# Optimization experiments

Hardware: AMD Instinct MI355X
Metric: run time of the kernel (lower is better)

## Reference

```python
import jax, jax.numpy as jnp
import numpy as np


def setup_inputs() -> dict:
    key = jax.random.key(0)
    ks = jax.random.split(key, 5)
    B, Td, Te, D, U = 8, 64, 1024, 256, 128
    scale = 1.0 / np.sqrt(D)
    return {
        "decoder_output": jax.random.normal(ks[0], (B, Td, D), jnp.float32),
        "encoder_output": jax.random.normal(ks[1], (B, Te, D), jnp.float32),
        "W1": jax.random.normal(ks[2], (D, U), jnp.float32) * scale,
        "b1": jnp.zeros((U,), jnp.float32),
        "W2": jax.random.normal(ks[3], (D, U), jnp.float32) * scale,
        "b2": jnp.zeros((U,), jnp.float32),
        "V": jax.random.normal(ks[4], (U, 1), jnp.float32) * (1.0 / np.sqrt(U)),
        "bV": jnp.zeros((1,), jnp.float32),
    }


def reference(decoder_output, encoder_output, W1, b1, W2, b2, V, bV):
    # Original loops over decoder timesteps (state unused) -> fully vectorized.
    # w_enc: [B,Te,U] computed ONCE (original wastefully recomputes per step;
    # math is identical).
    w_enc = jnp.einsum("bsd,du->bsu", encoder_output, W1) + b1
    w_dec = jnp.einsum("btd,du->btu", decoder_output, W2) + b2
    # additive score: [B,Td,Te]
    score = (
        jnp.einsum("btsu,u->bts", jnp.tanh(w_enc[:, None, :, :] + w_dec[:, :, None, :]), V[:, 0])
        + bV[0]
    )
    attn = jax.nn.softmax(score, axis=-1)  # softmax over encoder time
    context = jnp.einsum("bts,bsd->btd", attn, encoder_output)  # [B,Td,D]
    return context
```

## Files before the change

kernel.cpp:

```cpp
#include <hip/hip_runtime.h>
#include <math.h>

#define NB   8
#define TD   64
#define TE   1024
#define DDIM 256
#define UDIM 128
#define NSC  16
#define SCHUNK (TE / NSC)

__device__ __forceinline__ float rcp_fast(float x) {
    return __builtin_amdgcn_rcpf(x);
}

__global__ __launch_bounds__(256) void k_compute_E(
    const float* __restrict__ enc, const float* __restrict__ dec,
    const float* __restrict__ W1, const float* __restrict__ b1,
    const float* __restrict__ W2, const float* __restrict__ b2,
    float* __restrict__ E_enc, float* __restrict__ E_dec)
{
    __shared__ alignas(16) float ldsT[DDIM][20];

    const int blk = blockIdx.x;
    const float *W, *bias, *in;
    float *out;
    if (blk < 512) {
        in   = enc + (size_t)blk * 16 * DDIM;
        W    = W1;  bias = b1;
        out  = E_enc + (size_t)blk * 16 * UDIM;
    } else {
        const int bd = blk - 512;
        in   = dec + (size_t)bd * 16 * DDIM;
        W    = W2;  bias = b2;
        out  = E_dec + (size_t)bd * 16 * UDIM;
    }

    const int tid = threadIdx.x;
    for (int i = tid; i < 16 * DDIM; i += 256) {
        const int r = i >> 8;
        const int d = i & 255;
        ldsT[d][r] = in[i];
    }
    __syncthreads();

    const int u0 = (tid & 63) * 2;
    const int r0 = (tid >> 6) * 4;

    float acc[4][2];
    #pragma unroll
    for (int r = 0; r < 4; ++r) { acc[r][0] = 0.f; acc[r][1] = 0.f; }

    #pragma unroll 4
    for (int d = 0; d < DDIM; ++d) {
        const float2 w2 = *(const float2*)(W + d * UDIM + u0);
        const float4 a4 = *(const float4*)(&ldsT[d][r0]);
        acc[0][0] = fmaf(a4.x, w2.x, acc[0][0]); acc[0][1] = fmaf(a4.x, w2.y, acc[0][1]);
        acc[1][0] = fmaf(a4.y, w2.x, acc[1][0]); acc[1][1] = fmaf(a4.y, w2.y, acc[1][1]);
        acc[2][0] = fmaf(a4.z, w2.x, acc[2][0]); acc[2][1] = fmaf(a4.z, w2.y, acc[2][1]);
        acc[3][0] = fmaf(a4.w, w2.x, acc[3][0]); acc[3][1] = fmaf(a4.w, w2.y, acc[3][1]);
    }

    const float k2l2e = 2.0f * 1.4426950408889634f;
    const float bb0 = bias[u0], bb1 = bias[u0 + 1];
    #pragma unroll
    for (int r = 0; r < 4; ++r) {
        const float e0 = exp2f((acc[r][0] + bb0) * k2l2e);
        const float e1 = exp2f((acc[r][1] + bb1) * k2l2e);
        *(float2*)(out + (size_t)(r0 + r) * UDIM + u0) = make_float2(e0, e1);
    }
}

__global__ __launch_bounds__(1024) void k_score_softmax(
    const float* __restrict__ E_enc, const float* __restrict__ E_dec,
    const float* __restrict__ V, float* __restrict__ attn)
{
    __shared__ alignas(16) float et0[UDIM];
    __shared__ alignas(16) float et1[UDIM];
    __shared__ alignas(16) float mv[UDIM];
    __shared__ float redmax[16][2];
    __shared__ float redsum[16][2];

    const int blk = blockIdx.x;
    const int b   = blk >> 5;
    const int t0  = (blk & 31) * 2;
    const int tid = threadIdx.x;

    if (tid < UDIM)              et0[tid]          = E_dec[(size_t)(b * TD + t0) * UDIM + tid];
    else if (tid < 2 * UDIM)     et1[tid - UDIM]   = E_dec[(size_t)(b * TD + t0 + 1) * UDIM + (tid - UDIM)];
    else if (tid < 3 * UDIM)     mv[tid - 2*UDIM]  = -2.0f * V[tid - 2 * UDIM];
    __syncthreads();

    const int s = tid;
    const float* erow = E_enc + (size_t)(b * TE + s) * UDIM;

    float acc0 = 0.f, acc1 = 0.f;
    #pragma unroll 8
    for (int u = 0; u < UDIM; u += 4) {
        const float4 e  = *(const float4*)(erow + u);
        const float4 a0 = *(const float4*)(&et0[u]);
        const float4 a1 = *(const float4*)(&et1[u]);
        const float4 m  = *(const float4*)(&mv[u]);
        acc0 = fmaf(m.x, rcp_fast(fmaf(e.x, a0.x, 1.f)), acc0);
        acc1 = fmaf(m.x, rcp_fast(fmaf(e.x, a1.x, 1.f)), acc1);
        acc0 = fmaf(m.y, rcp_fast(fmaf(e.y, a0.y, 1.f)), acc0);
        acc1 = fmaf(m.y, rcp_fast(fmaf(e.y, a1.y, 1.f)), acc1);
        acc0 = fmaf(m.z, rcp_fast(fmaf(e.z, a0.z, 1.f)), acc0);
        acc1 = fmaf(m.z, rcp_fast(fmaf(e.z, a1.z, 1.f)), acc1);
        acc0 = fmaf(m.w, rcp_fast(fmaf(e.w, a0.w, 1.f)), acc0);
        acc1 = fmaf(m.w, rcp_fast(fmaf(e.w, a1.w, 1.f)), acc1);
    }

    float m0 = acc0, m1 = acc1;
    #pragma unroll
    for (int off = 32; off; off >>= 1) {
        m0 = fmaxf(m0, __shfl_xor(m0, off));
        m1 = fmaxf(m1, __shfl_xor(m1, off));
    }
    const int wv = tid >> 6;
    if ((tid & 63) == 0) { redmax[wv][0] = m0; redmax[wv][1] = m1; }
    __syncthreads();
    float gm0 = -3.4e38f, gm1 = -3.4e38f;
    #pragma unroll
    for (int i = 0; i < 16; ++i) {
        gm0 = fmaxf(gm0, redmax[i][0]);
        gm1 = fmaxf(gm1, redmax[i][1]);
    }

    const float p0 = __expf(acc0 - gm0);
    const float p1 = __expf(acc1 - gm1);

    float s0 = p0, s1 = p1;
    #pragma unroll
    for (int off = 32; off; off >>= 1) {
        s0 += __shfl_xor(s0, off);
        s1 += __shfl_xor(s1, off);
    }
    if ((tid & 63) == 0) { redsum[wv][0] = s0; redsum[wv][1] = s1; }
    __syncthreads();
    float gs0 = 0.f, gs1 = 0.f;
    #pragma unroll
    for (int i = 0; i < 16; ++i) { gs0 += redsum[i][0]; gs1 += redsum[i][1]; }

    attn[(size_t)(b * TD + t0)     * TE + s] = p0 * rcp_fast(gs0);
    attn[(size_t)(b * TD + t0 + 1) * TE + s] = p1 * rcp_fast(gs1);
}

__global__ __launch_bounds__(256) void k_context_part(
    const float* __restrict__ attn, const float* __restrict__ enc,
    float* __restrict__ part)
{
    __shared__ float al[16 * SCHUNK];

    const int blk = blockIdx.x;
    const int sc  = blk & 15;
    const int tg  = (blk >> 4) & 3;
    const int b   = blk >> 6;
    const int tid = threadIdx.x;
    const int t0  = tg * 16;
    const int s0  = sc * SCHUNK;

    for (int i = tid; i < 16 * SCHUNK; i += 256) {
        const int ti = i >> 6;
        const int si = i & 63;
        al[i] = attn[(size_t)(b * TD + t0 + ti) * TE + s0 + si];
    }
    __syncthreads();

    const int dq = tid & 63;   const int d0 = dq * 4;
    const int th = tid >> 6;

    float4 acc[4];
    #pragma unroll
    for (int j = 0; j < 4; ++j) acc[j] = make_float4(0.f, 0.f, 0.f, 0.f);

    for (int s = 0; s < SCHUNK; ++s) {
        const float4 e = *(const float4*)(enc + (size_t)(b * TE + s0 + s) * DDIM + d0);
        #pragma unroll
        for (int j = 0; j < 4; ++j) {
            const float a = al[(th * 4 + j) * SCHUNK + s];
            acc[j].x = fmaf(a, e.x, acc[j].x);
            acc[j].y = fmaf(a, e.y, acc[j].y);
            acc[j].z = fmaf(a, e.z, acc[j].z);
            acc[j].w = fmaf(a, e.w, acc[j].w);
        }
    }

    #pragma unroll
    for (int j = 0; j < 4; ++j) {
        const int t = t0 + th * 4 + j;
        *(float4*)(part + ((size_t)(b * TD + t) * NSC + sc) * DDIM + d0) = acc[j];
    }
}

__global__ __launch_bounds__(256) void k_reduce(
    const float* __restrict__ part, float* __restrict__ out)
{
    const int o  = blockIdx.x * 256 + threadIdx.x;
    const int d  = o & 255;
    const int bt = o >> 8;
    const float* p = part + (size_t)bt * NSC * DDIM + d;
    float s = 0.f;
    #pragma unroll
    for (int i = 0; i < NSC; ++i) s += p[(size_t)i * DDIM];
    out[o] = s;
}

extern "C" void kernel_launch(void* const* d_in, const int* in_sizes, int n_in,
                              void* d_out, int out_size, void* d_ws, size_t ws_size,
                              hipStream_t stream) {
    const float* dec = (const float*)d_in[0];
    const float* enc = (const float*)d_in[1];
    const float* W1  = (const float*)d_in[2];
    const float* b1  = (const float*)d_in[3];
    const float* W2  = (const float*)d_in[4];
    const float* b2  = (const float*)d_in[5];
    const float* V   = (const float*)d_in[6];

    float* ws    = (float*)d_ws;
    float* E_enc = ws;
    float* E_dec = E_enc + (size_t)NB * TE * UDIM;
    float* attn  = E_dec + (size_t)NB * TD * UDIM;
    float* part  = attn  + (size_t)NB * TD * TE;

    k_compute_E    <<<544, 256,  0, stream>>>(enc, dec, W1, b1, W2, b2, E_enc, E_dec);
    k_score_softmax<<<256, 1024, 0, stream>>>(E_enc, E_dec, V, attn);
    k_context_part <<<512, 256,  0, stream>>>(attn, enc, part);
    k_reduce       <<<512, 256,  0, stream>>>(part, (float*)d_out);
}
```

Before: 130.3 us.

## Fuse score, softmax, context and reduction into one kernel

Merges the score/softmax kernel with the context GEMV and the partial-sum reduction. Each block keeps its two softmax rows in shared memory, multiplies them against the encoder output for its batch, and reduces eight s-slices in LDS before writing the output. This removes the global round-trips for the attention matrix and the partial sums, plus two launches. In exchange, the context step now runs on only 256 blocks, and each block rereads the full encoder slice for just two decoder rows. The E_dec and V values are now read straight from global memory instead of being staged in LDS.

```diff
diff --git a/kernel.cpp b/kernel.cpp
--- a/kernel.cpp
+++ b/kernel.cpp
@@ -6,8 +6,6 @@
 #define TE   1024
 #define DDIM 256
 #define UDIM 128
-#define NSC  16
-#define SCHUNK (TE / NSC)
 
 __device__ __forceinline__ float rcp_fast(float x) {
     return __builtin_amdgcn_rcpf(x);
@@ -70,25 +68,24 @@
     }
 }
 
-__global__ __launch_bounds__(1024) void k_score_softmax(
+__global__ __launch_bounds__(1024) void k_fused(
     const float* __restrict__ E_enc, const float* __restrict__ E_dec,
-    const float* __restrict__ V, float* __restrict__ attn)
+    const float* __restrict__ V, const float* __restrict__ enc,
+    float* __restrict__ out)
 {
-    __shared__ alignas(16) float et0[UDIM];
-    __shared__ alignas(16) float et1[UDIM];
-    __shared__ alignas(16) float mv[UDIM];
-    __shared__ float redmax[16][2];
-    __shared__ float redsum[16][2];
+    __shared__ alignas(16) float pa[TE];
+    __shared__ alignas(16) float pb[TE];
+    __shared__ alignas(16) float red[8][2][DDIM];
+    __shared__ float redm[16][2];
+    __shared__ float reds[16][2];
 
     const int blk = blockIdx.x;
     const int b   = blk >> 5;
     const int t0  = (blk & 31) * 2;
     const int tid = threadIdx.x;
 
-    if (tid < UDIM)              et0[tid]          = E_dec[(size_t)(b * TD + t0) * UDIM + tid];
-    else if (tid < 2 * UDIM)     et1[tid - UDIM]   = E_dec[(size_t)(b * TD + t0 + 1) * UDIM + (tid - UDIM)];
-    else if (tid < 3 * UDIM)     mv[tid - 2*UDIM]  = -2.0f * V[tid - 2 * UDIM];
-    __syncthreads();
+    const float* er0 = E_dec + (size_t)(b * TD + t0) * UDIM;
+    const float* er1 = er0 + UDIM;
 
     const int s = tid;
     const float* erow = E_enc + (size_t)(b * TE + s) * UDIM;
@@ -97,18 +94,20 @@
     #pragma unroll 8
     for (int u = 0; u < UDIM; u += 4) {
         const float4 e  = *(const float4*)(erow + u);
-        const float4 a0 = *(const float4*)(&et0[u]);
-        const float4 a1 = *(const float4*)(&et1[u]);
-        const float4 m  = *(const float4*)(&mv[u]);
-        acc0 = fmaf(m.x, rcp_fast(fmaf(e.x, a0.x, 1.f)), acc0);
-        acc1 = fmaf(m.x, rcp_fast(fmaf(e.x, a1.x, 1.f)), acc1);
-        acc0 = fmaf(m.y, rcp_fast(fmaf(e.y, a0.y, 1.f)), acc0);
-        acc1 = fmaf(m.y, rcp_fast(fmaf(e.y, a1.y, 1.f)), acc1);
-        acc0 = fmaf(m.z, rcp_fast(fmaf(e.z, a0.z, 1.f)), acc0);
-        acc1 = fmaf(m.z, rcp_fast(fmaf(e.z, a1.z, 1.f)), acc1);
-        acc0 = fmaf(m.w, rcp_fast(fmaf(e.w, a0.w, 1.f)), acc0);
-        acc1 = fmaf(m.w, rcp_fast(fmaf(e.w, a1.w, 1.f)), acc1);
+        const float4 a0 = *(const float4*)(er0 + u);
+        const float4 a1 = *(const float4*)(er1 + u);
+        const float4 vv = *(const float4*)(V + u);
+        acc0 = fmaf(vv.x, rcp_fast(fmaf(e.x, a0.x, 1.f)), acc0);
+        acc1 = fmaf(vv.x, rcp_fast(fmaf(e.x, a1.x, 1.f)), acc1);
+        acc0 = fmaf(vv.y, rcp_fast(fmaf(e.y, a0.y, 1.f)), acc0);
+        acc1 = fmaf(vv.y, rcp_fast(fmaf(e.y, a1.y, 1.f)), acc1);
+        acc0 = fmaf(vv.z, rcp_fast(fmaf(e.z, a0.z, 1.f)), acc0);
+        acc1 = fmaf(vv.z, rcp_fast(fmaf(e.z, a1.z, 1.f)), acc1);
+        acc0 = fmaf(vv.w, rcp_fast(fmaf(e.w, a0.w, 1.f)), acc0);
+        acc1 = fmaf(vv.w, rcp_fast(fmaf(e.w, a1.w, 1.f)), acc1);
     }
+    acc0 *= -2.0f;
+    acc1 *= -2.0f;
 
     float m0 = acc0, m1 = acc1;
     #pragma unroll
@@ -117,13 +116,13 @@
         m1 = fmaxf(m1, __shfl_xor(m1, off));
     }
     const int wv = tid >> 6;
-    if ((tid & 63) == 0) { redmax[wv][0] = m0; redmax[wv][1] = m1; }
+    if ((tid & 63) == 0) { redm[wv][0] = m0; redm[wv][1] = m1; }
     __syncthreads();
     float gm0 = -3.4e38f, gm1 = -3.4e38f;
     #pragma unroll
     for (int i = 0; i < 16; ++i) {
-        gm0 = fmaxf(gm0, redmax[i][0]);
-        gm1 = fmaxf(gm1, redmax[i][1]);
+        gm0 = fmaxf(gm0, redm[i][0]);
+        gm1 = fmaxf(gm1, redm[i][1]);
     }
 
     const float p0 = __expf(acc0 - gm0);
@@ -135,74 +134,44 @@
         s0 += __shfl_xor(s0, off);
         s1 += __shfl_xor(s1, off);
     }
-    if ((tid & 63) == 0) { redsum[wv][0] = s0; redsum[wv][1] = s1; }
+    if ((tid & 63) == 0) { reds[wv][0] = s0; reds[wv][1] = s1; }
     __syncthreads();
     float gs0 = 0.f, gs1 = 0.f;
     #pragma unroll
-    for (int i = 0; i < 16; ++i) { gs0 += redsum[i][0]; gs1 += redsum[i][1]; }
+    for (int i = 0; i < 16; ++i) { gs0 += reds[i][0]; gs1 += reds[i][1]; }
 
-    attn[(size_t)(b * TD + t0)     * TE + s] = p0 * rcp_fast(gs0);
-    attn[(size_t)(b * TD + t0 + 1) * TE + s] = p1 * rcp_fast(gs1);
-}
-
-__global__ __launch_bounds__(256) void k_context_part(
-    const float* __restrict__ attn, const float* __restrict__ enc,
-    float* __restrict__ part)
-{
-    __shared__ float al[16 * SCHUNK];
-
-    const int blk = blockIdx.x;
-    const int sc  = blk & 15;
-    const int tg  = (blk >> 4) & 3;
-    const int b   = blk >> 6;
-    const int tid = threadIdx.x;
-    const int t0  = tg * 16;
-    const int s0  = sc * SCHUNK;
-
-    for (int i = tid; i < 16 * SCHUNK; i += 256) {
-        const int ti = i >> 6;
-        const int si = i & 63;
-        al[i] = attn[(size_t)(b * TD + t0 + ti) * TE + s0 + si];
-    }
+    pa[s] = p0 * rcp_fast(gs0);
+    pb[s] = p1 * rcp_fast(gs1);
     __syncthreads();
 
-    const int dq = tid & 63;   const int d0 = dq * 4;
-    const int th = tid >> 6;
+    const int dp = tid & 127;
+    const int d0 = dp * 2;
+    const int sq = tid >> 7;
+    const float* ebase = enc + ((size_t)(b * TE + sq * 128)) * DDIM + d0;
 
-    float4 acc[4];
-    #pragma unroll
-    for (int j = 0; j < 4; ++j) acc[j] = make_float4(0.f, 0.f, 0.f, 0.f);
+    float c00 = 0.f, c01 = 0.f, c10 = 0.f, c11 = 0.f;
+    #pragma unroll 4
+    for (int ss = 0; ss < 128; ++ss) {
+        const float a0 = pa[sq * 128 + ss];
+        const float a1 = pb[sq * 128 + ss];
+        const float2 e = *(const float2*)(ebase + (size_t)ss * DDIM);
+        c00 = fmaf(a0, e.x, c00);
+        c01 = fmaf(a0, e.y, c01);
+        c10 = fmaf(a1, e.x, c10);
+        c11 = fmaf(a1, e.y, c11);
+    }
+    *(float2*)(&red[sq][0][d0]) = make_float2(c00, c01);
+    *(float2*)(&red[sq][1][d0]) = make_float2(c10, c11);
+    __syncthreads();
 
-    for (int s = 0; s < SCHUNK; ++s) {
-        const float4 e = *(const float4*)(enc + (size_t)(b * TE + s0 + s) * DDIM + d0);
+    if (tid < 512) {
+        const int t = tid >> 8;
+        const int d = tid & 255;
+        float r = 0.f;
         #pragma unroll
-        for (int j = 0; j < 4; ++j) {
-            const float a = al[(th * 4 + j) * SCHUNK + s];
-            acc[j].x = fmaf(a, e.x, acc[j].x);
-            acc[j].y = fmaf(a, e.y, acc[j].y);
-            acc[j].z = fmaf(a, e.z, acc[j].z);
-            acc[j].w = fmaf(a, e.w, acc[j].w);
-        }
+        for (int q = 0; q < 8; ++q) r += red[q][t][d];
+        out[(size_t)(b * TD + t0 + t) * DDIM + d] = r;
     }
-
-    #pragma unroll
-    for (int j = 0; j < 4; ++j) {
-        const int t = t0 + th * 4 + j;
-        *(float4*)(part + ((size_t)(b * TD + t) * NSC + sc) * DDIM + d0) = acc[j];
-    }
-}
-
-__global__ __launch_bounds__(256) void k_reduce(
-    const float* __restrict__ part, float* __restrict__ out)
-{
-    const int o  = blockIdx.x * 256 + threadIdx.x;
-    const int d  = o & 255;
-    const int bt = o >> 8;
-    const float* p = part + (size_t)bt * NSC * DDIM + d;
-    float s = 0.f;
-    #pragma unroll
-    for (int i = 0; i < NSC; ++i) s += p[(size_t)i * DDIM];
-    out[o] = s;
 }
 
 extern "C" void kernel_launch(void* const* d_in, const int* in_sizes, int n_in,
@@ -219,11 +188,7 @@
     float* ws    = (float*)d_ws;
     float* E_enc = ws;
     float* E_dec = E_enc + (size_t)NB * TE * UDIM;
-    float* attn  = E_dec + (size_t)NB * TD * UDIM;
-    float* part  = attn  + (size_t)NB * TD * TE;
 
-    k_compute_E    <<<544, 256,  0, stream>>>(enc, dec, W1, b1, W2, b2, E_enc, E_dec);
-    k_score_softmax<<<256, 1024, 0, stream>>>(E_enc, E_dec, V, attn);
-    k_context_part <<<512, 256,  0, stream>>>(attn, enc, part);
-    k_reduce       <<<512, 256,  0, stream>>>(part, (float*)d_out);
+    k_compute_E<<<544, 256,  0, stream>>>(enc, dec, W1, b1, W2, b2, E_enc, E_dec);
+    k_fused    <<<256, 1024, 0, stream>>>(E_enc, E_dec, V, enc, (float*)d_out);
 }
```

Measured after the change: 131.1 us. About the same (+0.6%).
